# Performance work log

Measured on AMD Instinct MI355X. Metric: run time of the kernel, lower is better.

The kernel has to match this reference:

```python
import jax, jax.numpy as jnp
import numpy as np
import math

B, T, M, C, H = 2, 2048, 77, 512, 8
D = C // H  # head dim = 64


def setup_inputs() -> dict:
    key = jax.random.key(0)
    ks = jax.random.split(key, 20)
    s = 0.02
    inp = {
        "x": jax.random.normal(ks[0], (B, T, C), jnp.float32),
        "c": jax.random.normal(ks[1], (B, M, C), jnp.float32),
        # causal mask for self-attention (masked_fill where == 0)
        "attn_mask": jnp.tril(jnp.ones((T, T), jnp.int32))[None, None],
        "padding_mask": jnp.ones((B, M), jnp.int32),
    }
    names = ["Wq", "Wk", "Wv", "Wkc", "Wvc", "Wg1", "Wg2", "Wp"]
    for i, n in enumerate(names):
        inp[n] = jax.random.normal(ks[2 + i], (C, C), jnp.float32) * s
        inp["b" + n[1:]] = jnp.zeros((C,), jnp.float32)
    return inp


def _heads(t):
    # [B, S, C] -> [B, S, H, D]
    return t.reshape(t.shape[0], t.shape[1], H, D)


def reference(x, c, attn_mask, padding_mask,
              Wq, bq, Wk, bk, Wv, bv, Wkc, bkc, Wvc, bvc,
              Wg1, bg1, Wg2, bg2, Wp, bp):
    scale = 1.0 / math.sqrt(D)
    q = _heads(x @ Wq + bq)      # [B,T,H,D]
    k = _heads(x @ Wk + bk)      # [B,T,H,D]
    v = _heads(x @ Wv + bv)
    k_c = _heads(c @ Wkc + bkc)  # [B,M,H,D]
    v_c = _heads(c @ Wvc + bvc)

    # self-attention branch
    att = jnp.einsum("bthd,bshd->bhts", q, k) * scale   # [B,H,T,T]
    att = jnp.where(attn_mask == 0, -jnp.inf, att)
    att = jax.nn.softmax(att, axis=-1)
    y = jnp.einsum("bhts,bshd->bthd", att, v).reshape(B, T, C)

    # cross-attention branch to condition c
    att_c = jnp.einsum("bthd,bmhd->bhtm", q, k_c) * scale  # [B,H,T,M]
    att_c = jnp.where(padding_mask[:, None, None, :] == 0, -jnp.inf, att_c)
    att_c = jax.nn.softmax(att_c, axis=-1)
    y_c = jnp.einsum("bhtm,bmhd->bthd", att_c, v_c).reshape(B, T, C)

    # sigmoid gating fusion (note: gates cross-multiply branches, per source)
    gate_self = jax.nn.sigmoid(y @ Wg1 + bg1)
    gate_c = jax.nn.sigmoid(y_c @ Wg2 + bg2)
    y = gate_self * y_c + gate_c * y
    return y @ Wp + bp
```

## Files before the change

### kernel.cpp

```cpp
#include <hip/hip_runtime.h>
#include <hip/hip_bf16.h>
#include <math.h>

#define BB 2
#define TT 2048
#define MM 77
#define CC 512
#define HH 8
#define DD 64

typedef short bf16x8 __attribute__((ext_vector_type(8)));
typedef float f32x4  __attribute__((ext_vector_type(4)));

static __device__ __forceinline__ unsigned short f2bf(float x) {
    __hip_bfloat16 h = __float2bfloat16(x);
    return *reinterpret_cast<unsigned short*>(&h);
}
static __device__ __forceinline__ float bf2f(unsigned short u) {
    unsigned int v = ((unsigned int)u) << 16;
    return *reinterpret_cast<float*>(&v);
}

__global__ __launch_bounds__(256)
void wconv8(const float* __restrict__ w0, const float* __restrict__ w1,
            const float* __restrict__ w2, const float* __restrict__ w3,
            const float* __restrict__ w4, const float* __restrict__ w5,
            const float* __restrict__ w6, const float* __restrict__ w7,
            unsigned short* __restrict__ outbase)
{
    const float* W;
    switch (blockIdx.z) {
        case 0: W = w0; break; case 1: W = w1; break;
        case 2: W = w2; break; case 3: W = w3; break;
        case 4: W = w4; break; case 5: W = w5; break;
        case 6: W = w6; break; default: W = w7; break;
    }
    unsigned short* Wp = outbase + (size_t)blockIdx.z * 512 * 512;
    const int k0 = blockIdx.x * 64;
    const int n0 = blockIdx.y * 64;
    const int tid = threadIdx.x;
    __shared__ unsigned short t[64 * 72];

    #pragma unroll
    for (int it = 0; it < 4; ++it) {
        const int e = tid + 256 * it;
        const int r  = e >> 4;
        const int c4 = (e & 15) * 4;
        const float4 v = *(const float4*)(W + (size_t)(k0 + r) * 512 + n0 + c4);
        t[(c4 + 0) * 72 + r] = f2bf(v.x);
        t[(c4 + 1) * 72 + r] = f2bf(v.y);
        t[(c4 + 2) * 72 + r] = f2bf(v.z);
        t[(c4 + 3) * 72 + r] = f2bf(v.w);
    }
    __syncthreads();
    #pragma unroll
    for (int it = 0; it < 2; ++it) {
        const int e    = tid + 256 * it;
        const int gl   = e >> 7;
        const int ktl  = (e >> 6) & 1;
        const int lane = e & 63;
        const int l15  = lane & 15;
        const int q    = lane >> 4;
        const int4 v = *(const int4*)&t[(gl * 16 + l15) * 72 + ktl * 32 + q * 8];
        const int G  = (n0 >> 4) + gl;
        const int KT = (k0 >> 5) + ktl;
        *(int4*)(Wp + ((size_t)(G * 16 + KT) * 64 + lane) * 8) = v;
    }
}

__global__ __launch_bounds__(256)
void proj_all(const float* __restrict__ x, const float* __restrict__ cin,
              const unsigned short* __restrict__ Wt8,
              const float* __restrict__ bq, const float* __restrict__ bk,
              const float* __restrict__ bv, const float* __restrict__ bkc,
              const float* __restrict__ bvc,
              unsigned short* __restrict__ qb, unsigned short* __restrict__ kcb)
{
    __shared__ unsigned short As[2 * 16 * 64 * 8];

    const int tid = threadIdx.x;
    int b = blockIdx.x;
    const float* Ap; const unsigned short* Wtp;
    const float *bb0, *bb1, *bb2;
    unsigned short* outb;
    int row0, colb, N, S, whichStride;
    float oscale;
    if (b < 768) {
        row0 = (b & 127) * 32; colb = (b >> 7) * 256;
        Ap = x; Wtp = Wt8; N = BB * TT; S = TT;
        whichStride = 2097152; oscale = 0.125f;
        outb = qb; bb0 = bq; bb1 = bk; bb2 = bv;
    } else {
        b -= 768;
        row0 = (b % 5) * 32; colb = (b / 5) * 256;
        Ap = cin; Wtp = Wt8 + 3 * 262144; N = BB * MM; S = MM;
        whichStride = 131072; oscale = 1.0f;
        outb = kcb; bb0 = bkc; bb1 = bvc; bb2 = nullptr;
    }

    {
        const int r    = tid >> 3;
        const int rg   = r >> 4;
        const int l15r = r & 15;
        const int seg  = (tid & 7) * 64;
        const int gr   = row0 + r;
        unsigned short tmp[64];
        #pragma unroll
        for (int j = 0; j < 16; ++j) {
            float4 v = (gr < N) ? *(const float4*)(Ap + (size_t)gr * 512 + seg + j * 4)
                                : make_float4(0.f, 0.f, 0.f, 0.f);
            tmp[j*4+0] = f2bf(v.x); tmp[j*4+1] = f2bf(v.y);
            tmp[j*4+2] = f2bf(v.z); tmp[j*4+3] = f2bf(v.w);
        }
        #pragma unroll
        for (int jb = 0; jb < 8; ++jb) {
            const int k  = seg + jb * 8;
            const int kt = k >> 5;
            const int q  = (k >> 3) & 3;
            *(int4*)&As[((rg * 16 + kt) * 64 + q * 16 + l15r) * 8] = *(int4*)&tmp[jb*8];
        }
    }
    __syncthreads();

    const int wv   = tid >> 6;
    const int lane = tid & 63;
    const int l15  = lane & 15;
    const int quad = lane >> 4;
    const int wc   = colb + wv * 64;
    const int wcg  = wc >> 4;

    f32x4 acc[2][4];
    #pragma unroll
    for (int mi = 0; mi < 2; ++mi)
        #pragma unroll
        for (int ni = 0; ni < 4; ++ni) acc[mi][ni] = (f32x4){0.f, 0.f, 0.f, 0.f};

    bf16x8 b0v[4], b1v[4], b2v[4];
    #pragma unroll
    for (int ni = 0; ni < 4; ++ni) {
        b0v[ni] = *(const bf16x8*)(Wtp + (((size_t)(wcg + ni) * 16 + 0) << 9) + lane * 8);
        b1v[ni] = *(const bf16x8*)(Wtp + (((size_t)(wcg + ni) * 16 + 1) << 9) + lane * 8);
    }

    for (int kt = 0; kt < 16; ++kt) {
        if (kt + 2 < 16) {
            #pragma unroll
            for (int ni = 0; ni < 4; ++ni)
                b2v[ni] = *(const bf16x8*)(Wtp + (((size_t)(wcg + ni) * 16 + kt + 2) << 9) + lane * 8);
        }
        const bf16x8 a0 = *(const bf16x8*)&As[((0 * 16 + kt) * 64 + lane) * 8];
        const bf16x8 a1 = *(const bf16x8*)&As[((1 * 16 + kt) * 64 + lane) * 8];
        #pragma unroll
        for (int ni = 0; ni < 4; ++ni) {
            acc[0][ni] = __builtin_amdgcn_mfma_f32_16x16x32_bf16(a0, b0v[ni], acc[0][ni], 0, 0, 0);
            acc[1][ni] = __builtin_amdgcn_mfma_f32_16x16x32_bf16(a1, b0v[ni], acc[1][ni], 0, 0, 0);
        }
        #pragma unroll
        for (int ni = 0; ni < 4; ++ni) { b0v[ni] = b1v[ni]; b1v[ni] = b2v[ni]; }
    }

    const int which = wc >> 9;
    const float* bsel = (which == 0) ? bb0 : ((which == 1) ? bb1 : bb2);
    const float sc = (which == 0) ? oscale : 1.f;
    unsigned short* dst = outb + (size_t)which * whichStride;

    float bvv[4];
    #pragma unroll
    for (int ni = 0; ni < 4; ++ni)
        bvv[ni] = bsel[(wc + ni * 16 + l15) & 511];

    #pragma unroll
    for (int mi = 0; mi < 2; ++mi) {
        #pragma unroll
        for (int reg = 0; reg < 4; ++reg) {
            const int row = row0 + mi * 16 + quad * 4 + reg;
            if (row >= N) continue;
            const int b_ = row / S;
            const int s_ = row - b_ * S;
            #pragma unroll
            for (int ni = 0; ni < 4; ++ni) {
                const float v = (acc[mi][ni][reg] + bvv[ni]) * sc;
                const int cl = (wc + ni * 16 + l15) & 511;
                dst[((size_t)(b_ * HH + (cl >> 6)) * S + s_) * DD + (cl & 63)] = f2bf(v);
            }
        }
    }
}

template<int ACT, int OUT, int AMODE>
__global__ __launch_bounds__(256)
void gemm_rs(const void* __restrict__ A0, const void* __restrict__ A1,
             const void* __restrict__ A2, const void* __restrict__ A3,
             const unsigned short* __restrict__ Wt,
             const float* __restrict__ b0, const float* __restrict__ b1,
             void* __restrict__ out0, void* __restrict__ out1,
             int N, int NC)
{
    __shared__ unsigned short As[2 * 16 * 64 * 8];

    const int tid  = threadIdx.x;
    const int z    = blockIdx.z;
    const int row0 = blockIdx.x * 32;
    const int colb = blockIdx.y * 256;
    const void* Ap = z ? A1 : A0;

    {
        const int r    = tid >> 3;
        const int rg   = r >> 4;
        const int l15r = r & 15;
        const int seg  = (tid & 7) * 64;
        const int gr   = row0 + r;
        unsigned short tmp[64];
        if (AMODE == 2) {
            #pragma unroll
            for (int jb = 0; jb < 8; ++jb) {
                unsigned short a[8], bq_[8], c[8], d[8];
                if (gr < N) {
                    const size_t off = (size_t)gr * 512 + seg + jb * 8;
                    *(int4*)a   = *(const int4*)((const unsigned short*)A0 + off);
                    *(int4*)bq_ = *(const int4*)((const unsigned short*)A1 + off);
                    *(int4*)c   = *(const int4*)((const unsigned short*)A2 + off);
                    *(int4*)d   = *(const int4*)((const unsigned short*)A3 + off);
                    #pragma unroll
                    for (int k = 0; k < 8; ++k)
                        tmp[jb*8+k] = f2bf(bf2f(a[k]) * bf2f(bq_[k]) + bf2f(c[k]) * bf2f(d[k]));
                } else {
                    #pragma unroll
                    for (int k = 0; k < 8; ++k) tmp[jb*8+k] = 0;
                }
            }
        } else {
            const unsigned short* Ab = (const unsigned short*)Ap;
            #pragma unroll
            for (int jb = 0; jb < 8; ++jb) {
                int4 v = (gr < N) ? *(const int4*)(Ab + (size_t)gr * 512 + seg + jb * 8)
                                  : make_int4(0, 0, 0, 0);
                *(int4*)&tmp[jb*8] = v;
            }
        }
        #pragma unroll
        for (int jb = 0; jb < 8; ++jb) {
            const int k  = seg + jb * 8;
            const int kt = k >> 5;
            const int q  = (k >> 3) & 3;
            *(int4*)&As[((rg * 16 + kt) * 64 + q * 16 + l15r) * 8] = *(int4*)&tmp[jb*8];
        }
    }
    __syncthreads();

    const int wv   = tid >> 6;
    const int lane = tid & 63;
    const int l15  = lane & 15;
    const int quad = lane >> 4;
    const int wc   = colb + wv * 64;
    const int wcg  = wc >> 4;

    f32x4 acc[2][4];
    #pragma unroll
    for (int mi = 0; mi < 2; ++mi)
        #pragma unroll
        for (int ni = 0; ni < 4; ++ni) acc[mi][ni] = (f32x4){0.f, 0.f, 0.f, 0.f};

    const unsigned short* Wz = Wt + (size_t)z * NC;

    bf16x8 b0v[4], b1v[4], b2v[4];
    #pragma unroll
    for (int ni = 0; ni < 4; ++ni) {
        b0v[ni] = *(const bf16x8*)(Wz + (((size_t)(wcg + ni) * 16 + 0) << 9) + lane * 8);
        b1v[ni] = *(const bf16x8*)(Wz + (((size_t)(wcg + ni) * 16 + 1) << 9) + lane * 8);
    }

    for (int kt = 0; kt < 16; ++kt) {
        if (kt + 2 < 16) {
            #pragma unroll
            for (int ni = 0; ni < 4; ++ni)
                b2v[ni] = *(const bf16x8*)(Wz + (((size_t)(wcg + ni) * 16 + kt + 2) << 9) + lane * 8);
        }
        const bf16x8 a0 = *(const bf16x8*)&As[((0 * 16 + kt) * 64 + lane) * 8];
        const bf16x8 a1 = *(const bf16x8*)&As[((1 * 16 + kt) * 64 + lane) * 8];
        #pragma unroll
        for (int ni = 0; ni < 4; ++ni) {
            acc[0][ni] = __builtin_amdgcn_mfma_f32_16x16x32_bf16(a0, b0v[ni], acc[0][ni], 0, 0, 0);
            acc[1][ni] = __builtin_amdgcn_mfma_f32_16x16x32_bf16(a1, b0v[ni], acc[1][ni], 0, 0, 0);
        }
        #pragma unroll
        for (int ni = 0; ni < 4; ++ni) { b0v[ni] = b1v[ni]; b1v[ni] = b2v[ni]; }
    }

    const float* bsel = ((OUT == 1) && z) ? b1 : b0;
    float bvv[4];
    #pragma unroll
    for (int ni = 0; ni < 4; ++ni)
        bvv[ni] = bsel[(wc + ni * 16 + l15) & 511];

    #pragma unroll
    for (int mi = 0; mi < 2; ++mi) {
        #pragma unroll
        for (int reg = 0; reg < 4; ++reg) {
            const int row = row0 + mi * 16 + quad * 4 + reg;
            if (row >= N) continue;
            #pragma unroll
            for (int ni = 0; ni < 4; ++ni) {
                float v = acc[mi][ni][reg] + bvv[ni];
                if (ACT == 1) v = 1.f / (1.f + __expf(-v));
                const int col = wc + ni * 16 + l15;
                if (OUT == 0) {
                    ((float*)out0)[(size_t)row * 512 + col] = v;
                } else {
                    unsigned short* dst = (unsigned short*)(z ? out1 : out0);
                    dst[(size_t)row * 512 + col] = f2bf(v);
                }
            }
        }
    }
}

__global__ __launch_bounds__(256)
void transpose_all(const unsigned short* __restrict__ vin, unsigned short* __restrict__ vout,
                   const unsigned short* __restrict__ cin_, unsigned short* __restrict__ cout_)
{
    const int bx = blockIdx.x;
    const int bh = blockIdx.y;
    const unsigned short* in; unsigned short* outp;
    int S, W, s0;
    if (bx < 32) { in = vin;  outp = vout;  S = TT; W = TT;  s0 = bx * 64; }
    else         { in = cin_; outp = cout_; S = MM; W = 128; s0 = (bx - 32) * 64; }

    const int tid = threadIdx.x;
    __shared__ unsigned short t[64 * 80];

    #pragma unroll
    for (int it = 0; it < 2; ++it) {
        const int e = tid + 256 * it;
        const int row = e >> 3;
        const int blk = e & 7;
        int4 v = make_int4(0, 0, 0, 0);
        const int s = s0 + row;
        if (s < S) v = *(const int4*)(in + ((size_t)bh * S + s) * 64 + blk * 8);
        *(int4*)&t[row * 80 + ((blk ^ (row & 7)) * 8)] = v;
    }
    __syncthreads();
    #pragma unroll
    for (int it = 0; it < 2; ++it) {
        const int e = tid + 256 * it;
        const int d  = e >> 3;
        const int kb = e & 7;
        const int key0 = s0 + kb * 8;
        if (key0 < W) {
            unsigned short tmp[8];
            #pragma unroll
            for (int j = 0; j < 8; ++j) {
                const int kl = kb * 8 + j;
                tmp[j] = t[kl * 80 + (((d >> 3) ^ (kl & 7)) * 8) + (d & 7)];
            }
            *(int4*)(outp + ((size_t)bh * 64 + d) * W + key0) = *(int4*)tmp;
        }
    }
}

__global__ __launch_bounds__(256)
void attn_all(const unsigned short* __restrict__ Qh,
              const unsigned short* __restrict__ Kh,
              const unsigned short* __restrict__ Vth,
              unsigned short* __restrict__ yout,
              const unsigned short* __restrict__ Kch,
              const unsigned short* __restrict__ Vtch,
              unsigned short* __restrict__ ycout)
{
    int lin = blockIdx.x;
    int causal, S_kv, W, bh, qt;
    const unsigned short *Kb, *Vb;
    unsigned short* outp;
    if (lin < 512) {
        causal = 1; S_kv = TT; W = TT;
        bh = (lin & 7) | (((lin >> 3) & 1) << 3);
        const int qtr = lin >> 4;
        qt = (qtr < 16) ? (31 - qtr) : (qtr - 16);
        Kb = Kh + (size_t)bh * S_kv * 64;
        Vb = Vth + (size_t)bh * 64 * W;
        outp = yout;
    } else {
        lin -= 512;
        causal = 0; S_kv = MM; W = 128;
        bh = (lin & 7) | (((lin >> 3) & 1) << 3);
        qt = lin >> 4;
        Kb = Kch + (size_t)bh * S_kv * 64;
        Vb = Vtch + (size_t)bh * 64 * W;
        outp = ycout;
    }
    const int n_kt = causal ? (qt + 1) : 2;

    const int tid  = threadIdx.x;
    const int wv   = tid >> 6;
    const int lane = tid & 63;
    const int l15  = lane & 15;
    const int quad = lane >> 4;

    __shared__ unsigned short Ks[2][64 * 80];
    __shared__ unsigned short Vs[2][64 * 80];
    __shared__ unsigned short PT[4 * 16 * 72];

    const int t0 = qt * 64 + wv * 16;
    const unsigned short* qptr = Qh + ((size_t)bh * TT + t0 + l15) * 64 + quad * 8;
    const bf16x8 qb0 = *(const bf16x8*)(qptr);
    const bf16x8 qb1 = *(const bf16x8*)(qptr + 32);

    f32x4 Oacc[4];
    #pragma unroll
    for (int dt = 0; dt < 4; ++dt) Oacc[dt] = (f32x4){0.f, 0.f, 0.f, 0.f};
    float l = 0.f;

    int4 kR[2], vR[2];
    {
        #pragma unroll
        for (int it = 0; it < 2; ++it) {
            const int e = tid + 256 * it;
            const int row = e >> 3, blk = e & 7;
            kR[it] = (row < S_kv)
                ? *(const int4*)(Kb + (size_t)row * 64 + blk * 8) : make_int4(0,0,0,0);
            vR[it] = (blk * 8 < W)
                ? *(const int4*)(Vb + (size_t)row * W + blk * 8) : make_int4(0,0,0,0);
        }
        #pragma unroll
        for (int it = 0; it < 2; ++it) {
            const int e = tid + 256 * it;
            const int row = e >> 3, blk = e & 7;
            *(int4*)&Ks[0][row * 80 + ((blk ^ (row & 7)) * 8)] = kR[it];
            *(int4*)&Vs[0][row * 80 + ((blk ^ (row & 7)) * 8)] = vR[it];
        }
    }
    __syncthreads();

    for (int kt = 0; kt < n_kt; ++kt) {
        const int buf = kt & 1;
        const int s0 = kt * 64;

        if (kt + 1 < n_kt) {
            const int s1 = (kt + 1) * 64;
            #pragma unroll
            for (int it = 0; it < 2; ++it) {
                const int e = tid + 256 * it;
                const int row = e >> 3, blk = e & 7;
                const int s = s1 + row;
                kR[it] = (s < S_kv)
                    ? *(const int4*)(Kb + (size_t)s * 64 + blk * 8) : make_int4(0,0,0,0);
                vR[it] = (s1 + blk * 8 < W)
                    ? *(const int4*)(Vb + (size_t)row * W + s1 + blk * 8) : make_int4(0,0,0,0);
            }
        }

        f32x4 sacc[4];
        #pragma unroll
        for (int mt = 0; mt < 4; ++mt) {
            const int krow = 16 * mt + l15;
            const bf16x8 ka0 = *(const bf16x8*)&Ks[buf][krow * 80 + (((quad    ) ^ (krow & 7)) * 8)];
            const bf16x8 ka1 = *(const bf16x8*)&Ks[buf][krow * 80 + (((quad + 4) ^ (krow & 7)) * 8)];
            sacc[mt] = (f32x4){0.f, 0.f, 0.f, 0.f};
            sacc[mt] = __builtin_amdgcn_mfma_f32_16x16x32_bf16(ka0, qb0, sacc[mt], 0, 0, 0);
            sacc[mt] = __builtin_amdgcn_mfma_f32_16x16x32_bf16(ka1, qb1, sacc[mt], 0, 0, 0);
        }

        float sv[16];
        #pragma unroll
        for (int mt = 0; mt < 4; ++mt)
            #pragma unroll
            for (int reg = 0; reg < 4; ++reg)
                sv[mt * 4 + reg] = sacc[mt][reg];

        const bool cmask = (causal && kt == qt);
        if (cmask || (s0 + 64 > S_kv)) {
            const int lim = cmask ? (t0 + l15) : 0x7fffffff;
            #pragma unroll
            for (int mt = 0; mt < 4; ++mt)
                #pragma unroll
                for (int reg = 0; reg < 4; ++reg) {
                    const int kg = s0 + 16 * mt + quad * 4 + reg;
                    if (kg > lim || kg >= S_kv) sv[mt * 4 + reg] = -INFINITY;
                }
        }

        float p[16], psum = 0.f;
        #pragma unroll
        for (int i = 0; i < 16; ++i) { p[i] = __expf(sv[i]); psum += p[i]; }
        psum += __shfl_xor(psum, 16);
        psum += __shfl_xor(psum, 32);
        l += psum;

        unsigned short* ptw = &PT[wv * 16 * 72 + l15 * 72];
        #pragma unroll
        for (int mt = 0; mt < 4; ++mt) {
            ushort4 u;
            u.x = f2bf(p[mt * 4 + 0]); u.y = f2bf(p[mt * 4 + 1]);
            u.z = f2bf(p[mt * 4 + 2]); u.w = f2bf(p[mt * 4 + 3]);
            *(ushort4*)(ptw + 16 * mt + quad * 4) = u;
        }
        const bf16x8 pb0 = *(const bf16x8*)(ptw + quad * 8);
        const bf16x8 pb1 = *(const bf16x8*)(ptw + quad * 8 + 32);

        #pragma unroll
        for (int dt = 0; dt < 4; ++dt) {
            const int vrow = 16 * dt + l15;
            const bf16x8 va0 = *(const bf16x8*)&Vs[buf][vrow * 80 + (((quad    ) ^ (vrow & 7)) * 8)];
            const bf16x8 va1 = *(const bf16x8*)&Vs[buf][vrow * 80 + (((quad + 4) ^ (vrow & 7)) * 8)];
            Oacc[dt] = __builtin_amdgcn_mfma_f32_16x16x32_bf16(va0, pb0, Oacc[dt], 0, 0, 0);
            Oacc[dt] = __builtin_amdgcn_mfma_f32_16x16x32_bf16(va1, pb1, Oacc[dt], 0, 0, 0);
        }

        if (kt + 1 < n_kt) {
            const int nbuf = buf ^ 1;
            #pragma unroll
            for (int it = 0; it < 2; ++it) {
                const int e = tid + 256 * it;
                const int row = e >> 3, blk = e & 7;
                *(int4*)&Ks[nbuf][row * 80 + ((blk ^ (row & 7)) * 8)] = kR[it];
                *(int4*)&Vs[nbuf][row * 80 + ((blk ^ (row & 7)) * 8)] = vR[it];
            }
        }
        __syncthreads();
    }

    const int b = bh >> 3, h = bh & 7;
    const float inv_l = 1.f / l;
    const int t = t0 + l15;
    unsigned short* ob = outp + ((size_t)b * TT + t) * CC + h * DD + quad * 4;
    #pragma unroll
    for (int dt = 0; dt < 4; ++dt) {
        ushort4 u;
        u.x = f2bf(Oacc[dt][0] * inv_l);
        u.y = f2bf(Oacc[dt][1] * inv_l);
        u.z = f2bf(Oacc[dt][2] * inv_l);
        u.w = f2bf(Oacc[dt][3] * inv_l);
        *(ushort4*)(ob + 16 * dt) = u;
    }
}

extern "C" void kernel_launch(void* const* d_in, const int* in_sizes, int n_in,
                              void* d_out, int out_size, void* d_ws, size_t ws_size,
                              hipStream_t stream)
{
    const float* x   = (const float*)d_in[0];
    const float* cin = (const float*)d_in[1];
    const float* Wq  = (const float*)d_in[4];   const float* bq  = (const float*)d_in[5];
    const float* Wk  = (const float*)d_in[6];   const float* bk  = (const float*)d_in[7];
    const float* Wv  = (const float*)d_in[8];   const float* bv  = (const float*)d_in[9];
    const float* Wkc = (const float*)d_in[10];  const float* bkc = (const float*)d_in[11];
    const float* Wvc = (const float*)d_in[12];  const float* bvc = (const float*)d_in[13];
    const float* Wg1 = (const float*)d_in[14];  const float* bg1 = (const float*)d_in[15];
    const float* Wg2 = (const float*)d_in[16];  const float* bg2 = (const float*)d_in[17];
    const float* Wp  = (const float*)d_in[18];  const float* bp  = (const float*)d_in[19];

    float* out = (float*)d_out;
    char*  w   = (char*)d_ws;
    const size_t MB = 1024 * 1024;

    unsigned short* Wt8  = (unsigned short*)(w);
    unsigned short* qb   = (unsigned short*)(w + 4  * MB);
    unsigned short* kb   = (unsigned short*)(w + 8  * MB);
    unsigned short* vb   = (unsigned short*)(w + 12 * MB);
    unsigned short* vtb  = (unsigned short*)(w + 16 * MB);
    unsigned short* yb   = (unsigned short*)(w + 20 * MB);
    unsigned short* ycb  = (unsigned short*)(w + 24 * MB);
    unsigned short* g1b  = (unsigned short*)(w + 28 * MB);
    unsigned short* g2b  = (unsigned short*)(w + 32 * MB);
    unsigned short* kcb  = (unsigned short*)(w + 40 * MB);
    unsigned short* vcb  = (unsigned short*)(w + 40 * MB + 256 * 1024);
    unsigned short* vtcb = (unsigned short*)(w + 40 * MB + 512 * 1024);

    const dim3 blk(256);

    wconv8<<<dim3(8, 8, 8), blk, 0, stream>>>(Wq, Wk, Wv, Wkc, Wvc, Wg1, Wg2, Wp, Wt8);

    proj_all<<<dim3(788), blk, 0, stream>>>(
        x, cin, Wt8, bq, bk, bv, bkc, bvc, qb, kcb);

    transpose_all<<<dim3(34, BB * HH), blk, 0, stream>>>(vb, vtb, vcb, vtcb);

    attn_all<<<dim3(1024), blk, 0, stream>>>(qb, kb, vtb, yb, kcb, vtcb, ycb);

    gemm_rs<1, 1, 0><<<dim3(128, 2, 2), blk, 0, stream>>>(
        yb, ycb, nullptr, nullptr, Wt8 + 5 * 262144, bg1, bg2, g1b, g2b,
        BB * TT, 262144);

    gemm_rs<0, 0, 2><<<dim3(128, 2), blk, 0, stream>>>(
        g1b, ycb, g2b, yb, Wt8 + 7 * 262144, bp, nullptr, out, nullptr,
        BB * TT, 0);
}
```

Before: 202.6 us.

## Fuse gate GEMMs and output projection into one kernel, single-buffer attention K/V

Replaces the two gemm_rs launches (sigmoid gate GEMMs, then the gated-combine plus output projection) with a single gatesproj kernel. Each block holds 16 rows of y, y_c and both gate results in shared memory, so the g1/g2 intermediates never go to global memory. The attention kernel also drops K/V double buffering in LDS and adds an extra barrier per tile, which lowers shared-memory use but exposes more synchronization. The fused kernel uses only 256 blocks of 16 rows, and each wave runs a long serial loop over columns, so parallelism per block is reduced.

```diff
diff --git a/kernel.cpp b/kernel.cpp
--- a/kernel.cpp
+++ b/kernel.cpp
@@ -182,134 +182,6 @@
                 const float v = (acc[mi][ni][reg] + bvv[ni]) * sc;
                 const int cl = (wc + ni * 16 + l15) & 511;
                 dst[((size_t)(b_ * HH + (cl >> 6)) * S + s_) * DD + (cl & 63)] = f2bf(v);
-            }
-        }
-    }
-}
-
-template<int ACT, int OUT, int AMODE>
-__global__ __launch_bounds__(256)
-void gemm_rs(const void* __restrict__ A0, const void* __restrict__ A1,
-             const void* __restrict__ A2, const void* __restrict__ A3,
-             const unsigned short* __restrict__ Wt,
-             const float* __restrict__ b0, const float* __restrict__ b1,
-             void* __restrict__ out0, void* __restrict__ out1,
-             int N, int NC)
-{
-    __shared__ unsigned short As[2 * 16 * 64 * 8];
-
-    const int tid  = threadIdx.x;
-    const int z    = blockIdx.z;
-    const int row0 = blockIdx.x * 32;
-    const int colb = blockIdx.y * 256;
-    const void* Ap = z ? A1 : A0;
-
-    {
-        const int r    = tid >> 3;
-        const int rg   = r >> 4;
-        const int l15r = r & 15;
-        const int seg  = (tid & 7) * 64;
-        const int gr   = row0 + r;
-        unsigned short tmp[64];
-        if (AMODE == 2) {
-            #pragma unroll
-            for (int jb = 0; jb < 8; ++jb) {
-                unsigned short a[8], bq_[8], c[8], d[8];
-                if (gr < N) {
-                    const size_t off = (size_t)gr * 512 + seg + jb * 8;
-                    *(int4*)a   = *(const int4*)((const unsigned short*)A0 + off);
-                    *(int4*)bq_ = *(const int4*)((const unsigned short*)A1 + off);
-                    *(int4*)c   = *(const int4*)((const unsigned short*)A2 + off);
-                    *(int4*)d   = *(const int4*)((const unsigned short*)A3 + off);
-                    #pragma unroll
-                    for (int k = 0; k < 8; ++k)
-                        tmp[jb*8+k] = f2bf(bf2f(a[k]) * bf2f(bq_[k]) + bf2f(c[k]) * bf2f(d[k]));
-                } else {
-                    #pragma unroll
-                    for (int k = 0; k < 8; ++k) tmp[jb*8+k] = 0;
-                }
-            }
-        } else {
-            const unsigned short* Ab = (const unsigned short*)Ap;
-            #pragma unroll
-            for (int jb = 0; jb < 8; ++jb) {
-                int4 v = (gr < N) ? *(const int4*)(Ab + (size_t)gr * 512 + seg + jb * 8)
-                                  : make_int4(0, 0, 0, 0);
-                *(int4*)&tmp[jb*8] = v;
-            }
-        }
-        #pragma unroll
-        for (int jb = 0; jb < 8; ++jb) {
-            const int k  = seg + jb * 8;
-            const int kt = k >> 5;
-            const int q  = (k >> 3) & 3;
-            *(int4*)&As[((rg * 16 + kt) * 64 + q * 16 + l15r) * 8] = *(int4*)&tmp[jb*8];
-        }
-    }
-    __syncthreads();
-
-    const int wv   = tid >> 6;
-    const int lane = tid & 63;
-    const int l15  = lane & 15;
-    const int quad = lane >> 4;
-    const int wc   = colb + wv * 64;
-    const int wcg  = wc >> 4;
-
-    f32x4 acc[2][4];
-    #pragma unroll
-    for (int mi = 0; mi < 2; ++mi)
-        #pragma unroll
-        for (int ni = 0; ni < 4; ++ni) acc[mi][ni] = (f32x4){0.f, 0.f, 0.f, 0.f};
-
-    const unsigned short* Wz = Wt + (size_t)z * NC;
-
-    bf16x8 b0v[4], b1v[4], b2v[4];
-    #pragma unroll
-    for (int ni = 0; ni < 4; ++ni) {
-        b0v[ni] = *(const bf16x8*)(Wz + (((size_t)(wcg + ni) * 16 + 0) << 9) + lane * 8);
-        b1v[ni] = *(const bf16x8*)(Wz + (((size_t)(wcg + ni) * 16 + 1) << 9) + lane * 8);
-    }
-
-    for (int kt = 0; kt < 16; ++kt) {
-        if (kt + 2 < 16) {
-            #pragma unroll
-            for (int ni = 0; ni < 4; ++ni)
-                b2v[ni] = *(const bf16x8*)(Wz + (((size_t)(wcg + ni) * 16 + kt + 2) << 9) + lane * 8);
-        }
-        const bf16x8 a0 = *(const bf16x8*)&As[((0 * 16 + kt) * 64 + lane) * 8];
-        const bf16x8 a1 = *(const bf16x8*)&As[((1 * 16 + kt) * 64 + lane) * 8];
-        #pragma unroll
-        for (int ni = 0; ni < 4; ++ni) {
-            acc[0][ni] = __builtin_amdgcn_mfma_f32_16x16x32_bf16(a0, b0v[ni], acc[0][ni], 0, 0, 0);
-            acc[1][ni] = __builtin_amdgcn_mfma_f32_16x16x32_bf16(a1, b0v[ni], acc[1][ni], 0, 0, 0);
-        }
-        #pragma unroll
-        for (int ni = 0; ni < 4; ++ni) { b0v[ni] = b1v[ni]; b1v[ni] = b2v[ni]; }
-    }
-
-    const float* bsel = ((OUT == 1) && z) ? b1 : b0;
-    float bvv[4];
-    #pragma unroll
-    for (int ni = 0; ni < 4; ++ni)
-        bvv[ni] = bsel[(wc + ni * 16 + l15) & 511];
-
-    #pragma unroll
-    for (int mi = 0; mi < 2; ++mi) {
-        #pragma unroll
-        for (int reg = 0; reg < 4; ++reg) {
-            const int row = row0 + mi * 16 + quad * 4 + reg;
-            if (row >= N) continue;
-            #pragma unroll
-            for (int ni = 0; ni < 4; ++ni) {
-                float v = acc[mi][ni][reg] + bvv[ni];
-                if (ACT == 1) v = 1.f / (1.f + __expf(-v));
-                const int col = wc + ni * 16 + l15;
-                if (OUT == 0) {
-                    ((float*)out0)[(size_t)row * 512 + col] = v;
-                } else {
-                    unsigned short* dst = (unsigned short*)(z ? out1 : out0);
-                    dst[(size_t)row * 512 + col] = f2bf(v);
-                }
             }
         }
     }
@@ -396,8 +268,8 @@
     const int l15  = lane & 15;
     const int quad = lane >> 4;
 
-    __shared__ unsigned short Ks[2][64 * 80];
-    __shared__ unsigned short Vs[2][64 * 80];
+    __shared__ unsigned short Ks[64 * 80];
+    __shared__ unsigned short Vs[64 * 80];
     __shared__ unsigned short PT[4 * 16 * 72];
 
     const int t0 = qt * 64 + wv * 16;
@@ -425,14 +297,13 @@
         for (int it = 0; it < 2; ++it) {
             const int e = tid + 256 * it;
             const int row = e >> 3, blk = e & 7;
-            *(int4*)&Ks[0][row * 80 + ((blk ^ (row & 7)) * 8)] = kR[it];
-            *(int4*)&Vs[0][row * 80 + ((blk ^ (row & 7)) * 8)] = vR[it];
+            *(int4*)&Ks[row * 80 + ((blk ^ (row & 7)) * 8)] = kR[it];
+            *(int4*)&Vs[row * 80 + ((blk ^ (row & 7)) * 8)] = vR[it];
         }
     }
     __syncthreads();
 
     for (int kt = 0; kt < n_kt; ++kt) {
-        const int buf = kt & 1;
         const int s0 = kt * 64;
 
         if (kt + 1 < n_kt) {
@@ -453,8 +324,8 @@
         #pragma unroll
         for (int mt = 0; mt < 4; ++mt) {
             const int krow = 16 * mt + l15;
-            const bf16x8 ka0 = *(const bf16x8*)&Ks[buf][krow * 80 + (((quad    ) ^ (krow & 7)) * 8)];
-            const bf16x8 ka1 = *(const bf16x8*)&Ks[buf][krow * 80 + (((quad + 4) ^ (krow & 7)) * 8)];
+            const bf16x8 ka0 = *(const bf16x8*)&Ks[krow * 80 + (((quad    ) ^ (krow & 7)) * 8)];
+            const bf16x8 ka1 = *(const bf16x8*)&Ks[krow * 80 + (((quad + 4) ^ (krow & 7)) * 8)];
             sacc[mt] = (f32x4){0.f, 0.f, 0.f, 0.f};
             sacc[mt] = __builtin_amdgcn_mfma_f32_16x16x32_bf16(ka0, qb0, sacc[mt], 0, 0, 0);
             sacc[mt] = __builtin_amdgcn_mfma_f32_16x16x32_bf16(ka1, qb1, sacc[mt], 0, 0, 0);
@@ -500,23 +371,23 @@
         #pragma unroll
         for (int dt = 0; dt < 4; ++dt) {
             const int vrow = 16 * dt + l15;
-            const bf16x8 va0 = *(const bf16x8*)&Vs[buf][vrow * 80 + (((quad    ) ^ (vrow & 7)) * 8)];
-            const bf16x8 va1 = *(const bf16x8*)&Vs[buf][vrow * 80 + (((quad + 4) ^ (vrow & 7)) * 8)];
+            const bf16x8 va0 = *(const bf16x8*)&Vs[vrow * 80 + (((quad    ) ^ (vrow & 7)) * 8)];
+            const bf16x8 va1 = *(const bf16x8*)&Vs[vrow * 80 + (((quad + 4) ^ (vrow & 7)) * 8)];
             Oacc[dt] = __builtin_amdgcn_mfma_f32_16x16x32_bf16(va0, pb0, Oacc[dt], 0, 0, 0);
             Oacc[dt] = __builtin_amdgcn_mfma_f32_16x16x32_bf16(va1, pb1, Oacc[dt], 0, 0, 0);
         }
 
         if (kt + 1 < n_kt) {
-            const int nbuf = buf ^ 1;
+            __syncthreads();
             #pragma unroll
             for (int it = 0; it < 2; ++it) {
                 const int e = tid + 256 * it;
                 const int row = e >> 3, blk = e & 7;
-                *(int4*)&Ks[nbuf][row * 80 + ((blk ^ (row & 7)) * 8)] = kR[it];
-                *(int4*)&Vs[nbuf][row * 80 + ((blk ^ (row & 7)) * 8)] = vR[it];
-            }
-        }
-        __syncthreads();
+                *(int4*)&Ks[row * 80 + ((blk ^ (row & 7)) * 8)] = kR[it];
+                *(int4*)&Vs[row * 80 + ((blk ^ (row & 7)) * 8)] = vR[it];
+            }
+            __syncthreads();
+        }
     }
 
     const int b = bh >> 3, h = bh & 7;
@@ -531,6 +402,156 @@
         u.z = f2bf(Oacc[dt][2] * inv_l);
         u.w = f2bf(Oacc[dt][3] * inv_l);
         *(ushort4*)(ob + 16 * dt) = u;
+    }
+}
+
+__global__ __launch_bounds__(256)
+void gatesproj(const unsigned short* __restrict__ yb,
+               const unsigned short* __restrict__ ycb,
+               const unsigned short* __restrict__ Wt8,
+               const float* __restrict__ bg1, const float* __restrict__ bg2,
+               const float* __restrict__ bp, float* __restrict__ out)
+{
+    __shared__ unsigned short Ys[16 * 512];
+    __shared__ unsigned short Cs[16 * 512];
+    __shared__ unsigned short G1s[16 * 512];
+    __shared__ unsigned short G2s[16 * 512];
+
+    const int tid  = threadIdx.x;
+    const int row0 = blockIdx.x * 16;
+    const int wv   = tid >> 6;
+    const int lane = tid & 63;
+    const int l15  = lane & 15;
+    const int quad = lane >> 4;
+
+    {
+        const int r    = tid & 15;
+        const int kseg = (tid >> 4) * 32;
+        const size_t base = (size_t)(row0 + r) * 512 + kseg;
+        #pragma unroll
+        for (int jb = 0; jb < 4; ++jb) {
+            const int k  = kseg + jb * 8;
+            const int kt = k >> 5;
+            const int q  = (k >> 3) & 3;
+            const int di = (kt * 64 + q * 16 + r) * 8;
+            *(int4*)&Ys[di] = *(const int4*)(yb  + base + jb * 8);
+            *(int4*)&Cs[di] = *(const int4*)(ycb + base + jb * 8);
+        }
+    }
+    __syncthreads();
+
+    {
+        const int gsel = wv >> 1;
+        const unsigned short* Wsel = Wt8 + (size_t)(5 + gsel) * 262144;
+        const unsigned short* Asrc = gsel ? Cs : Ys;
+        const float* bsel = gsel ? bg2 : bg1;
+        unsigned short* Gdst = gsel ? G2s : G1s;
+        const int colbase = (wv & 1) * 256;
+
+        for (int t = 0; t < 4; ++t) {
+            const int ct  = colbase + t * 64;
+            const int wcg = ct >> 4;
+            f32x4 acc[4];
+            #pragma unroll
+            for (int ni = 0; ni < 4; ++ni) acc[ni] = (f32x4){0.f, 0.f, 0.f, 0.f};
+
+            bf16x8 b0v[4], b1v[4], b2v[4];
+            #pragma unroll
+            for (int ni = 0; ni < 4; ++ni) {
+                b0v[ni] = *(const bf16x8*)(Wsel + (((size_t)(wcg + ni) * 16 + 0) << 9) + lane * 8);
+                b1v[ni] = *(const bf16x8*)(Wsel + (((size_t)(wcg + ni) * 16 + 1) << 9) + lane * 8);
+            }
+            for (int kt = 0; kt < 16; ++kt) {
+                if (kt + 2 < 16) {
+                    #pragma unroll
+                    for (int ni = 0; ni < 4; ++ni)
+                        b2v[ni] = *(const bf16x8*)(Wsel + (((size_t)(wcg + ni) * 16 + kt + 2) << 9) + lane * 8);
+                }
+                const bf16x8 a = *(const bf16x8*)&Asrc[(kt * 64 + lane) * 8];
+                #pragma unroll
+                for (int ni = 0; ni < 4; ++ni)
+                    acc[ni] = __builtin_amdgcn_mfma_f32_16x16x32_bf16(a, b0v[ni], acc[ni], 0, 0, 0);
+                #pragma unroll
+                for (int ni = 0; ni < 4; ++ni) { b0v[ni] = b1v[ni]; b1v[ni] = b2v[ni]; }
+            }
+            #pragma unroll
+            for (int ni = 0; ni < 4; ++ni) {
+                const int c = ct + ni * 16 + l15;
+                const float bb = bsel[c];
+                #pragma unroll
+                for (int reg = 0; reg < 4; ++reg) {
+                    float v = acc[ni][reg] + bb;
+                    v = 1.f / (1.f + __expf(-v));
+                    const int m = quad * 4 + reg;
+                    Gdst[((c >> 5) * 64 + ((c >> 3) & 3) * 16 + m) * 8 + (c & 7)] = f2bf(v);
+                }
+            }
+        }
+    }
+    __syncthreads();
+
+    {
+        const unsigned short* Wp8 = Wt8 + (size_t)7 * 262144;
+        const int ct0 = wv * 128;
+        f32x4 acc[2][4];
+        #pragma unroll
+        for (int t = 0; t < 2; ++t)
+            #pragma unroll
+            for (int ni = 0; ni < 4; ++ni) acc[t][ni] = (f32x4){0.f, 0.f, 0.f, 0.f};
+
+        bf16x8 b0v[2][4], b1v[2][4], b2v[2][4];
+        #pragma unroll
+        for (int t = 0; t < 2; ++t)
+            #pragma unroll
+            for (int ni = 0; ni < 4; ++ni) {
+                const int wcg = (ct0 + t * 64) >> 4;
+                b0v[t][ni] = *(const bf16x8*)(Wp8 + (((size_t)(wcg + ni) * 16 + 0) << 9) + lane * 8);
+                b1v[t][ni] = *(const bf16x8*)(Wp8 + (((size_t)(wcg + ni) * 16 + 1) << 9) + lane * 8);
+            }
+
+        for (int kt = 0; kt < 16; ++kt) {
+            if (kt + 2 < 16) {
+                #pragma unroll
+                for (int t = 0; t < 2; ++t)
+                    #pragma unroll
+                    for (int ni = 0; ni < 4; ++ni) {
+                        const int wcg = (ct0 + t * 64) >> 4;
+                        b2v[t][ni] = *(const bf16x8*)(Wp8 + (((size_t)(wcg + ni) * 16 + kt + 2) << 9) + lane * 8);
+                    }
+            }
+            const int ai = (kt * 64 + lane) * 8;
+            unsigned short g1v[8], ccv[8], g2v[8], yyv[8], zf[8];
+            *(int4*)g1v = *(const int4*)&G1s[ai];
+            *(int4*)ccv = *(const int4*)&Cs[ai];
+            *(int4*)g2v = *(const int4*)&G2s[ai];
+            *(int4*)yyv = *(const int4*)&Ys[ai];
+            #pragma unroll
+            for (int j = 0; j < 8; ++j)
+                zf[j] = f2bf(bf2f(g1v[j]) * bf2f(ccv[j]) + bf2f(g2v[j]) * bf2f(yyv[j]));
+            const bf16x8 a = *(const bf16x8*)zf;
+            #pragma unroll
+            for (int t = 0; t < 2; ++t)
+                #pragma unroll
+                for (int ni = 0; ni < 4; ++ni)
+                    acc[t][ni] = __builtin_amdgcn_mfma_f32_16x16x32_bf16(a, b0v[t][ni], acc[t][ni], 0, 0, 0);
+            #pragma unroll
+            for (int t = 0; t < 2; ++t)
+                #pragma unroll
+                for (int ni = 0; ni < 4; ++ni) { b0v[t][ni] = b1v[t][ni]; b1v[t][ni] = b2v[t][ni]; }
+        }
+
+        #pragma unroll
+        for (int t = 0; t < 2; ++t)
+            #pragma unroll
+            for (int ni = 0; ni < 4; ++ni) {
+                const int col = ct0 + t * 64 + ni * 16 + l15;
+                const float bb = bp[col];
+                #pragma unroll
+                for (int reg = 0; reg < 4; ++reg) {
+                    const int row = row0 + quad * 4 + reg;
+                    out[(size_t)row * 512 + col] = acc[t][ni][reg] + bb;
+                }
+            }
     }
 }
 
@@ -560,8 +581,6 @@
     unsigned short* vtb  = (unsigned short*)(w + 16 * MB);
     unsigned short* yb   = (unsigned short*)(w + 20 * MB);
     unsigned short* ycb  = (unsigned short*)(w + 24 * MB);
-    unsigned short* g1b  = (unsigned short*)(w + 28 * MB);
-    unsigned short* g2b  = (unsigned short*)(w + 32 * MB);
     unsigned short* kcb  = (unsigned short*)(w + 40 * MB);
     unsigned short* vcb  = (unsigned short*)(w + 40 * MB + 256 * 1024);
     unsigned short* vtcb = (unsigned short*)(w + 40 * MB + 512 * 1024);
@@ -577,11 +596,5 @@
 
     attn_all<<<dim3(1024), blk, 0, stream>>>(qb, kb, vtb, yb, kcb, vtcb, ycb);
 
-    gemm_rs<1, 1, 0><<<dim3(128, 2, 2), blk, 0, stream>>>(
-        yb, ycb, nullptr, nullptr, Wt8 + 5 * 262144, bg1, bg2, g1b, g2b,
-        BB * TT, 262144);
-
-    gemm_rs<0, 0, 2><<<dim3(128, 2), blk, 0, stream>>>(
-        g1b, ycb, g2b, yb, Wt8 + 7 * 262144, bp, nullptr, out, nullptr,
-        BB * TT, 0);
-}
+    gatesproj<<<dim3(256), blk, 0, stream>>>(yb, ycb, Wt8, bg1, bg2, bp, out);
+}
```

New measurement: 204.9 us. Within noise of the previous version (+1.1%).
